# Performance work log

Measured on AMD Instinct MI355X. Metric: run time of the kernel, lower is better.

## Reference

```python
import jax, jax.numpy as jnp
import numpy as np

N_NODES = 100000
N_EDGES = 3200000
IN_C = 256
HID = 32
OUT_C = 64


def setup_inputs() -> dict:
    key = jax.random.key(0)
    ks = jax.random.split(key, 12)
    x = jax.random.normal(ks[0], (N_NODES, IN_C), dtype=jnp.float32)
    edge_index = jax.random.randint(ks[1], (2, N_EDGES), 0, N_NODES, dtype=jnp.int64)

    def lin(kw, kb, fan_in, fan_out):
        bound = 1.0 / np.sqrt(fan_in)
        W = jax.random.uniform(kw, (fan_out, fan_in), jnp.float32, -bound, bound)
        b = jax.random.uniform(kb, (fan_out,), jnp.float32, -bound, bound)
        return W, b

    W0, b0 = lin(ks[2], ks[3], IN_C, HID)
    W1, b1 = lin(ks[4], ks[5], HID, HID)
    W2, b2 = lin(ks[6], ks[7], HID, HID)
    W3, b3 = lin(ks[8], ks[9], HID, HID)
    W4, b4 = lin(ks[10], ks[11], HID, OUT_C)
    return {"x": x, "edge_index": edge_index,
            "W0": W0, "b0": b0, "W1": W1, "b1": b1, "W2": W2, "b2": b2,
            "W3": W3, "b3": b3, "W4": W4, "b4": b4}


def _gcn_norm(edge_index, num_nodes):
    # add self loops, symmetric normalization (PyG gcn_norm, edge_weight = 1)
    loop = jnp.arange(num_nodes, dtype=edge_index.dtype)
    row = jnp.concatenate([edge_index[0], loop])  # source nodes
    col = jnp.concatenate([edge_index[1], loop])  # target nodes
    deg = jax.ops.segment_sum(jnp.ones_like(col, dtype=jnp.float32), col,
                              num_segments=num_nodes)
    dinv = jnp.where(deg > 0, jax.lax.rsqrt(jnp.maximum(deg, 1e-12)), 0.0)
    norm = dinv[row] * dinv[col]
    return row, col, norm


def reference(x, edge_index, W0, b0, W1, b1, W2, b2, W3, b3, W4, b4):
    row, col, norm = _gcn_norm(edge_index, N_NODES)

    def prop(h):
        # gather source features, scale by norm, scatter-add to targets
        return jax.ops.segment_sum(norm[:, None] * h[row], col,
                                   num_segments=N_NODES)

    def sgconv(h, W, b):  # SGConv with K=1: propagate then linear
        return prop(h) @ W.T + b

    h = x @ W0.T + b0
    h = jax.nn.relu(sgconv(h, W1, b1))
    h = jax.nn.relu(sgconv(h, W2, b2))
    h = jax.nn.relu(sgconv(h, W3, b3))
    return h @ W4.T + b4
```

## Files before the change

kernel.cpp:

```cpp
#include <hip/hip_runtime.h>
#include <hip/hip_fp16.h>

#define N_NODES 100000
#define N_EDGES 3200000
#define IN_C 256
#define HID 32
#define OUT_C 64
#define CAP 80
#define NP 100032
#define BINW 256
#define BSH 8
#define NBIN 391
#define BCHUNK 4096
#define CAPB 12288

typedef _Float16 f16x8 __attribute__((ext_vector_type(8)));
typedef float f32x4 __attribute__((ext_vector_type(4)));

__device__ __forceinline__ float dot4(const float4 a, const float4 b) {
    return a.x * b.x + a.y * b.y + a.z * b.z + a.w * b.w;
}

__device__ __forceinline__ float4 h4tof4(uint2 v) {
    __half2 a = *reinterpret_cast<__half2*>(&v.x);
    __half2 b = *reinterpret_cast<__half2*>(&v.y);
    float2 fa = __half22float2(a), fb = __half22float2(b);
    return make_float4(fa.x, fa.y, fb.x, fb.y);
}
__device__ __forceinline__ uint2 f4toh4(float4 f) {
    __half2 a = __float22half2_rn(make_float2(f.x, f.y));
    __half2 b = __float22half2_rn(make_float2(f.z, f.w));
    uint2 v;
    v.x = *reinterpret_cast<unsigned int*>(&a);
    v.y = *reinterpret_cast<unsigned int*>(&b);
    return v;
}

__device__ __forceinline__ void h8acc(uint4 v, float* acc) {
    __half2* p = reinterpret_cast<__half2*>(&v);
    #pragma unroll
    for (int i = 0; i < 4; ++i) {
        float2 f = __half22float2(p[i]);
        acc[2 * i] += f.x;
        acc[2 * i + 1] += f.y;
    }
}

__device__ __forceinline__ unsigned packh2(_Float16 a, _Float16 b) {
    unsigned short ua = __builtin_bit_cast(unsigned short, a);
    unsigned short ub = __builtin_bit_cast(unsigned short, b);
    return (unsigned)ua | ((unsigned)ub << 16);
}


__global__ __launch_bounds__(256) void k_binscatter(const int* __restrict__ row,
                                                    const int* __restrict__ col,
                                                    int* __restrict__ binCursor,
                                                    unsigned* __restrict__ pairs) {
    __shared__ int lcnt[512];
    __shared__ int lofs[512];
    __shared__ int gbase[512];
    __shared__ int sbuf[2][256];
    __shared__ unsigned stage[BCHUNK];
    __shared__ unsigned short sbin[BCHUNK];
    const int t = threadIdx.x;
    for (int i = t; i < 512; i += 256) lcnt[i] = 0;
    __syncthreads();

    const int e0 = blockIdx.x * BCHUNK;
    const int e1 = min(N_EDGES, e0 + BCHUNK);
    const int cn = e1 - e0;

    for (int i = e0 + t; i < e1; i += 256)
        atomicAdd(&lcnt[col[i] >> BSH], 1);
    __syncthreads();

    const int a0 = lcnt[2 * t], a1 = lcnt[2 * t + 1];
    sbuf[0][t] = a0 + a1;
    __syncthreads();
    int s = 0;
    for (int off = 1; off < 256; off <<= 1) {
        int d = s ^ 1;
        int v = sbuf[s][t];
        if (t >= off) v += sbuf[s][t - off];
        sbuf[d][t] = v;
        __syncthreads();
        s = d;
    }
    const int excl = sbuf[s][t] - (a0 + a1);
    lofs[2 * t] = excl;
    lofs[2 * t + 1] = excl + a0;
    __syncthreads();

    for (int i = t; i < 512; i += 256) {
        int c = lcnt[i];
        gbase[i] = c ? atomicAdd(&binCursor[i], c) : 0;
        lcnt[i] = 0;
    }
    __syncthreads();

    for (int i = e0 + t; i < e1; i += 256) {
        int cc = col[i];
        int b = cc >> BSH;
        int p = lofs[b] + atomicAdd(&lcnt[b], 1);
        stage[p] = ((unsigned)row[i] << 8) | (unsigned)(cc & 255);
        sbin[p] = (unsigned short)b;
    }
    __syncthreads();

    for (int i = t; i < cn; i += 256) {
        int b = sbin[i];
        int pos = gbase[b] + (i - lofs[b]);
        if (pos < CAPB)
            pairs[(size_t)b * CAPB + pos] = stage[i];
    }
}

__global__ __launch_bounds__(256) void k_binbuild(const unsigned* __restrict__ pairs,
                                                  const int* __restrict__ binCursor,
                                                  int* __restrict__ bucket,
                                                  int* __restrict__ degc,
                                                  float* __restrict__ dinv) {
    __shared__ int cur[BINW];
    const int t = threadIdx.x;
    const int bin = blockIdx.x;
    const int base = bin * BINW;
    cur[t] = 0;
    __syncthreads();
    const unsigned* __restrict__ slab = pairs + (size_t)bin * CAPB;
    const int cn = min(binCursor[bin], CAPB);
    for (int i = t; i < cn; i += 256) {
        unsigned p = slab[i];
        int c = (int)(p & 255u);
        int pos = atomicAdd(&cur[c], 1);
        if (pos < CAP) bucket[(size_t)(base + c) * CAP + pos] = (int)(p >> 8);
    }
    __syncthreads();
    int n = base + t;
    if (n < N_NODES) {
        int d = cur[t];
        degc[n] = d;
        dinv[n] = 1.0f / sqrtf((float)(d + 1));
    }
}


__global__ void k_hist(const int* __restrict__ col, int* __restrict__ deg) {
    int i = blockIdx.x * 256 + threadIdx.x;
    if (i < N_EDGES) atomicAdd(&deg[col[i]], 1);
}

__global__ void k_scan1(const int* __restrict__ deg, int* __restrict__ rowptr,
                        int* __restrict__ bsum) {
    __shared__ int buf[2][1024];
    const int t = threadIdx.x, b = blockIdx.x;
    const int i = b * 1024 + t;
    int v = (i < N_NODES) ? deg[i] : 0;
    buf[0][t] = v;
    __syncthreads();
    int src = 0;
    for (int off = 1; off < 1024; off <<= 1) {
        int dst = src ^ 1;
        int val = buf[src][t];
        if (t >= off) val += buf[src][t - off];
        buf[dst][t] = val;
        __syncthreads();
        src = dst;
    }
    int incl = buf[src][t];
    if (i < N_NODES) rowptr[i] = incl - v;
    if (t == 1023) bsum[b] = incl;
}

__global__ void k_scan2(int* __restrict__ bsum, int nb) {
    __shared__ int buf[2][128];
    const int t = threadIdx.x;
    int v = (t < nb) ? bsum[t] : 0;
    buf[0][t] = v;
    __syncthreads();
    int src = 0;
    for (int off = 1; off < 128; off <<= 1) {
        int dst = src ^ 1;
        int val = buf[src][t];
        if (t >= off) val += buf[src][t - off];
        buf[dst][t] = val;
        __syncthreads();
        src = dst;
    }
    if (t < nb) bsum[t] = buf[src][t] - v;
}

__global__ void k_scan3(int* __restrict__ rowptr, const int* __restrict__ bsum) {
    int i = blockIdx.x * 256 + threadIdx.x;
    if (i < N_NODES) rowptr[i] += bsum[i >> 10];
}

__global__ void k_dinv(const int* __restrict__ cnt, int stride,
                       float* __restrict__ dinv, int* __restrict__ degc) {
    int i = blockIdx.x * 256 + threadIdx.x;
    if (i < N_NODES) {
        int d = cnt[i * stride];
        degc[i] = d;
        dinv[i] = 1.0f / sqrtf((float)(d + 1));
    }
}

__global__ void k_scatter(const int* __restrict__ row, const int* __restrict__ col,
                          const int* __restrict__ rowptr, int* __restrict__ cursor,
                          int* __restrict__ csr) {
    int i = blockIdx.x * 256 + threadIdx.x;
    if (i < N_EDGES) {
        int c = col[i];
        int pos = rowptr[c] + atomicAdd(&cursor[c], 1);
        csr[pos] = row[i];
    }
}

__global__ __launch_bounds__(256) void k_lin0_mfma(
        const float* __restrict__ x,
        const float* __restrict__ W0,
        const float* __restrict__ b0,
        const float* __restrict__ dinv,
        uint2* __restrict__ g2) {
    __shared__ f16x8 WH[1024];
    __shared__ f16x8 WL[1024];

    const int t = threadIdx.x;
    const int w = t >> 6;
    const int l = t & 63;
    const int lr = l & 15;
    const int lg = l >> 4;

    for (int s = t; s < 1024; s += 256) {
        const int lane = s & 63;
        const int mtks = s >> 6;
        const int ks = mtks & 7, mt = mtks >> 3;
        const float* wr = W0 + (size_t)(mt * 16 + (lane & 15)) * IN_C
                             + ks * 32 + (lane >> 4) * 8;
        float4 a0 = *(const float4*)(wr);
        float4 a1 = *(const float4*)(wr + 4);
        float v[8] = {a0.x, a0.y, a0.z, a0.w, a1.x, a1.y, a1.z, a1.w};
        f16x8 h, lo;
        #pragma unroll
        for (int e = 0; e < 8; ++e) {
            float sv = v[e] * 16.0f;
            _Float16 hh = (_Float16)sv;
            h[e] = hh;
            lo[e] = (_Float16)(sv - (float)hh);
        }
        WH[s] = h;
        WL[s] = lo;
    }
    __syncthreads();

    const int unit = blockIdx.x * 4 + w;
    if (unit * 32 >= N_NODES) return;
    const int n0 = unit * 32;

    f32x4 acc[2][2];
    #pragma unroll
    for (int mt = 0; mt < 2; ++mt)
        #pragma unroll
        for (int nt = 0; nt < 2; ++nt)
            acc[mt][nt] = (f32x4){0.f, 0.f, 0.f, 0.f};

    const float* xr0 = x + (size_t)(n0 + lr) * IN_C + lg * 8;
    const float* xr1 = x + (size_t)(n0 + 16 + lr) * IN_C + lg * 8;

    #pragma unroll
    for (int ks = 0; ks < 8; ++ks) {
        float4 u0 = *(const float4*)(xr0 + ks * 32);
        float4 u1 = *(const float4*)(xr0 + ks * 32 + 4);
        float4 v0 = *(const float4*)(xr1 + ks * 32);
        float4 v1 = *(const float4*)(xr1 + ks * 32 + 4);
        float fu[8] = {u0.x, u0.y, u0.z, u0.w, u1.x, u1.y, u1.z, u1.w};
        float fv[8] = {v0.x, v0.y, v0.z, v0.w, v1.x, v1.y, v1.z, v1.w};
        f16x8 xh0, xl0, xh1, xl1;
        #pragma unroll
        for (int e = 0; e < 8; ++e) {
            _Float16 h0 = (_Float16)fu[e];
            xh0[e] = h0;
            xl0[e] = (_Float16)(fu[e] - (float)h0);
            _Float16 h1 = (_Float16)fv[e];
            xh1[e] = h1;
            xl1[e] = (_Float16)(fv[e] - (float)h1);
        }
        #pragma unroll
        for (int mt = 0; mt < 2; ++mt) {
            f16x8 wh = WH[mt * 512 + ks * 64 + l];
            f16x8 wl = WL[mt * 512 + ks * 64 + l];
            acc[mt][0] = __builtin_amdgcn_mfma_f32_16x16x32_f16(wh, xh0, acc[mt][0], 0, 0, 0);
            acc[mt][0] = __builtin_amdgcn_mfma_f32_16x16x32_f16(wh, xl0, acc[mt][0], 0, 0, 0);
            acc[mt][0] = __builtin_amdgcn_mfma_f32_16x16x32_f16(wl, xh0, acc[mt][0], 0, 0, 0);
            acc[mt][1] = __builtin_amdgcn_mfma_f32_16x16x32_f16(wh, xh1, acc[mt][1], 0, 0, 0);
            acc[mt][1] = __builtin_amdgcn_mfma_f32_16x16x32_f16(wh, xl1, acc[mt][1], 0, 0, 0);
            acc[mt][1] = __builtin_amdgcn_mfma_f32_16x16x32_f16(wl, xh1, acc[mt][1], 0, 0, 0);
        }
    }

    #pragma unroll
    for (int nt = 0; nt < 2; ++nt) {
        const int node = n0 + nt * 16 + lr;
        const float dv = dinv[node];
        #pragma unroll
        for (int mt = 0; mt < 2; ++mt) {
            const float4 bb = *(const float4*)(b0 + mt * 16 + lg * 4);
            f32x4 a = acc[mt][nt];
            float4 r = make_float4((a[0] * 0.0625f + bb.x) * dv,
                                   (a[1] * 0.0625f + bb.y) * dv,
                                   (a[2] * 0.0625f + bb.z) * dv,
                                   (a[3] * 0.0625f + bb.w) * dv);
            g2[(size_t)node * 8 + mt * 4 + lg] = f4toh4(r);
        }
    }
}

__global__ __launch_bounds__(256) void k_prop_mfma(
        const uint2* __restrict__ g2, const int* __restrict__ idx,
        const int* __restrict__ cnt_arr,
        const float* __restrict__ dinv,
        const float* __restrict__ W, const float* __restrict__ b,
        uint2* __restrict__ gout2) {
    __shared__ f16x8 WH[128], WL[128];
    const int t = threadIdx.x;
    if (t < 128) {
        const int lane = t & 63, mt = t >> 6;
        const float* wr = W + (size_t)(mt * 16 + (lane & 15)) * HID + (lane >> 4) * 8;
        f16x8 h, lo;
        #pragma unroll
        for (int e = 0; e < 8; ++e) {
            float sv = wr[e] * 8.0f;
            _Float16 hh = (_Float16)sv;
            h[e] = hh;
            lo[e] = (_Float16)(sv - (float)hh);
        }
        WH[t] = h;
        WL[t] = lo;
    }
    __syncthreads();

    const int l = t & 63;
    const int tile = blockIdx.x * 4 + (t >> 6);
    const int n0 = tile * 16;
    if (n0 >= N_NODES) return;
    const int node = n0 + (l & 15);
    const int lg = l >> 4;

    const uint4* __restrict__ g4 = (const uint4*)g2;
    float acc[8];
    #pragma unroll
    for (int i = 0; i < 8; ++i) acc[i] = 0.f;
    h8acc(g4[(size_t)node * 4 + lg], acc);

    const int cn = min(cnt_arr[node], CAP);
    const int* __restrict__ e = idx + (size_t)node * CAP;
    int j = 0;
    for (; j + 8 <= cn; j += 8) {
        int4 ra = *(const int4*)(e + j);
        int4 rb = *(const int4*)(e + j + 4);
        uint4 v0 = g4[(size_t)ra.x * 4 + lg];
        uint4 v1 = g4[(size_t)ra.y * 4 + lg];
        uint4 v2 = g4[(size_t)ra.z * 4 + lg];
        uint4 v3 = g4[(size_t)ra.w * 4 + lg];
        uint4 v4 = g4[(size_t)rb.x * 4 + lg];
        uint4 v5 = g4[(size_t)rb.y * 4 + lg];
        uint4 v6 = g4[(size_t)rb.z * 4 + lg];
        uint4 v7 = g4[(size_t)rb.w * 4 + lg];
        h8acc(v0, acc); h8acc(v1, acc); h8acc(v2, acc); h8acc(v3, acc);
        h8acc(v4, acc); h8acc(v5, acc); h8acc(v6, acc); h8acc(v7, acc);
    }
    for (; j < cn; ++j) h8acc(g4[(size_t)e[j] * 4 + lg], acc);

    f16x8 bh, bl;
    #pragma unroll
    for (int i = 0; i < 8; ++i) {
        _Float16 hh = (_Float16)acc[i];
        bh[i] = hh;
        bl[i] = (_Float16)(acc[i] - (float)hh);
    }

    f32x4 c0 = (f32x4){0.f, 0.f, 0.f, 0.f};
    f32x4 c1 = (f32x4){0.f, 0.f, 0.f, 0.f};
    {
        f16x8 wh0 = WH[l], wl0 = WL[l];
        f16x8 wh1 = WH[64 + l], wl1 = WL[64 + l];
        c0 = __builtin_amdgcn_mfma_f32_16x16x32_f16(wh0, bh, c0, 0, 0, 0);
        c0 = __builtin_amdgcn_mfma_f32_16x16x32_f16(wh0, bl, c0, 0, 0, 0);
        c0 = __builtin_amdgcn_mfma_f32_16x16x32_f16(wl0, bh, c0, 0, 0, 0);
        c1 = __builtin_amdgcn_mfma_f32_16x16x32_f16(wh1, bh, c1, 0, 0, 0);
        c1 = __builtin_amdgcn_mfma_f32_16x16x32_f16(wh1, bl, c1, 0, 0, 0);
        c1 = __builtin_amdgcn_mfma_f32_16x16x32_f16(wl1, bh, c1, 0, 0, 0);
    }

    const float dv = dinv[node];
    #pragma unroll
    for (int mt = 0; mt < 2; ++mt) {
        const f32x4 bb = *(const f32x4*)(b + mt * 16 + lg * 4);
        f32x4 a = mt ? c1 : c0;
        float4 r;
        r.x = fmaxf(bb[0] + dv * (a[0] * 0.125f), 0.f) * dv;
        r.y = fmaxf(bb[1] + dv * (a[1] * 0.125f), 0.f) * dv;
        r.z = fmaxf(bb[2] + dv * (a[2] * 0.125f), 0.f) * dv;
        r.w = fmaxf(bb[3] + dv * (a[3] * 0.125f), 0.f) * dv;
        gout2[(size_t)node * 8 + mt * 4 + lg] = f4toh4(r);
    }
}

__global__ __launch_bounds__(256) void k_last_mfma(
        const uint2* __restrict__ g2, const int* __restrict__ idx,
        const int* __restrict__ cnt_arr,
        const float* __restrict__ dinv,
        const float* __restrict__ W3, const float* __restrict__ b3,
        const float* __restrict__ W4, const float* __restrict__ b4,
        float4* __restrict__ out4) {
    __shared__ f16x8 WH3[128], WL3[128];
    __shared__ f16x8 WH4[256], WL4[256];
    const int t = threadIdx.x;
    if (t < 128) {
        const int lane = t & 63, mt = t >> 6;
        const float* wr = W3 + (size_t)(mt * 16 + (lane & 15)) * HID + (lane >> 4) * 8;
        f16x8 h, lo;
        #pragma unroll
        for (int e = 0; e < 8; ++e) {
            float sv = wr[e] * 8.0f;
            _Float16 hh = (_Float16)sv;
            h[e] = hh;
            lo[e] = (_Float16)(sv - (float)hh);
        }
        WH3[t] = h;
        WL3[t] = lo;
    }
    {
        const int lane = t & 63, mt = t >> 6;
        const float* wr = W4 + (size_t)(mt * 16 + (lane & 15)) * HID + (lane >> 4) * 8;
        f16x8 h, lo;
        #pragma unroll
        for (int e = 0; e < 8; ++e) {
            float sv = wr[e] * 8.0f;
            _Float16 hh = (_Float16)sv;
            h[e] = hh;
            lo[e] = (_Float16)(sv - (float)hh);
        }
        WH4[t] = h;
        WL4[t] = lo;
    }
    __syncthreads();

    const int l = t & 63;
    const int tile = blockIdx.x * 4 + (t >> 6);
    const int n0 = tile * 16;
    if (n0 >= N_NODES) return;
    const int nl = l & 15;
    const int node = n0 + nl;
    const int lg = l >> 4;

    const uint4* __restrict__ g4 = (const uint4*)g2;
    float acc[8];
    #pragma unroll
    for (int i = 0; i < 8; ++i) acc[i] = 0.f;
    h8acc(g4[(size_t)node * 4 + lg], acc);

    const int cn = min(cnt_arr[node], CAP);
    const int* __restrict__ e = idx + (size_t)node * CAP;
    int j = 0;
    for (; j + 8 <= cn; j += 8) {
        int4 ra = *(const int4*)(e + j);
        int4 rb = *(const int4*)(e + j + 4);
        uint4 v0 = g4[(size_t)ra.x * 4 + lg];
        uint4 v1 = g4[(size_t)ra.y * 4 + lg];
        uint4 v2 = g4[(size_t)ra.z * 4 + lg];
        uint4 v3 = g4[(size_t)ra.w * 4 + lg];
        uint4 v4 = g4[(size_t)rb.x * 4 + lg];
        uint4 v5 = g4[(size_t)rb.y * 4 + lg];
        uint4 v6 = g4[(size_t)rb.z * 4 + lg];
        uint4 v7 = g4[(size_t)rb.w * 4 + lg];
        h8acc(v0, acc); h8acc(v1, acc); h8acc(v2, acc); h8acc(v3, acc);
        h8acc(v4, acc); h8acc(v5, acc); h8acc(v6, acc); h8acc(v7, acc);
    }
    for (; j < cn; ++j) h8acc(g4[(size_t)e[j] * 4 + lg], acc);

    f16x8 bh, bl;
    #pragma unroll
    for (int i = 0; i < 8; ++i) {
        _Float16 hh = (_Float16)acc[i];
        bh[i] = hh;
        bl[i] = (_Float16)(acc[i] - (float)hh);
    }

    f32x4 c0 = (f32x4){0.f, 0.f, 0.f, 0.f};
    f32x4 c1 = (f32x4){0.f, 0.f, 0.f, 0.f};
    {
        f16x8 wh0 = WH3[l], wl0 = WL3[l];
        f16x8 wh1 = WH3[64 + l], wl1 = WL3[64 + l];
        c0 = __builtin_amdgcn_mfma_f32_16x16x32_f16(wh0, bh, c0, 0, 0, 0);
        c0 = __builtin_amdgcn_mfma_f32_16x16x32_f16(wh0, bl, c0, 0, 0, 0);
        c0 = __builtin_amdgcn_mfma_f32_16x16x32_f16(wl0, bh, c0, 0, 0, 0);
        c1 = __builtin_amdgcn_mfma_f32_16x16x32_f16(wh1, bh, c1, 0, 0, 0);
        c1 = __builtin_amdgcn_mfma_f32_16x16x32_f16(wh1, bl, c1, 0, 0, 0);
        c1 = __builtin_amdgcn_mfma_f32_16x16x32_f16(wl1, bh, c1, 0, 0, 0);
    }

    const float dv = dinv[node];
    const f32x4 b3a = *(const f32x4*)(b3 + lg * 4);
    const f32x4 b3b = *(const f32x4*)(b3 + 16 + lg * 4);
    float h0[4], h1[4];
    #pragma unroll
    for (int r = 0; r < 4; ++r) {
        h0[r] = fmaxf(b3a[r] + dv * (c0[r] * 0.125f), 0.f);
        h1[r] = fmaxf(b3b[r] + dv * (c1[r] * 0.125f), 0.f);
    }

    unsigned ph[2][2], pl_[2][2];
    #pragma unroll
    for (int p = 0; p < 2; ++p) {
        _Float16 a0 = (_Float16)h0[2 * p], a1 = (_Float16)h0[2 * p + 1];
        _Float16 l0 = (_Float16)(h0[2 * p] - (float)a0);
        _Float16 l1 = (_Float16)(h0[2 * p + 1] - (float)a1);
        ph[0][p] = packh2(a0, a1);
        pl_[0][p] = packh2(l0, l1);
        _Float16 c0_ = (_Float16)h1[2 * p], c1_ = (_Float16)h1[2 * p + 1];
        _Float16 d0 = (_Float16)(h1[2 * p] - (float)c0_);
        _Float16 d1 = (_Float16)(h1[2 * p + 1] - (float)c1_);
        ph[1][p] = packh2(c0_, c1_);
        pl_[1][p] = packh2(d0, d1);
    }

    union { unsigned u[4]; f16x8 v; } Bh, Bl;
    #pragma unroll
    for (int q = 0; q < 4; ++q) {
        int src = nl + 16 * ((lg & 1) * 2 + (q >> 1));
        unsigned a0 = (unsigned)__shfl((int)ph[0][q & 1], src, 64);
        unsigned a1 = (unsigned)__shfl((int)ph[1][q & 1], src, 64);
        Bh.u[q] = (lg >= 2) ? a1 : a0;
        unsigned c0_ = (unsigned)__shfl((int)pl_[0][q & 1], src, 64);
        unsigned c1_ = (unsigned)__shfl((int)pl_[1][q & 1], src, 64);
        Bl.u[q] = (lg >= 2) ? c1_ : c0_;
    }

    f32x4 o0 = (f32x4){0.f, 0.f, 0.f, 0.f};
    f32x4 o1 = (f32x4){0.f, 0.f, 0.f, 0.f};
    f32x4 o2 = (f32x4){0.f, 0.f, 0.f, 0.f};
    f32x4 o3 = (f32x4){0.f, 0.f, 0.f, 0.f};
    {
        f16x8 wh, wl;
        wh = WH4[l];        wl = WL4[l];
        o0 = __builtin_amdgcn_mfma_f32_16x16x32_f16(wh, Bh.v, o0, 0, 0, 0);
        o0 = __builtin_amdgcn_mfma_f32_16x16x32_f16(wh, Bl.v, o0, 0, 0, 0);
        o0 = __builtin_amdgcn_mfma_f32_16x16x32_f16(wl, Bh.v, o0, 0, 0, 0);
        wh = WH4[64 + l];   wl = WL4[64 + l];
        o1 = __builtin_amdgcn_mfma_f32_16x16x32_f16(wh, Bh.v, o1, 0, 0, 0);
        o1 = __builtin_amdgcn_mfma_f32_16x16x32_f16(wh, Bl.v, o1, 0, 0, 0);
        o1 = __builtin_amdgcn_mfma_f32_16x16x32_f16(wl, Bh.v, o1, 0, 0, 0);
        wh = WH4[128 + l];  wl = WL4[128 + l];
        o2 = __builtin_amdgcn_mfma_f32_16x16x32_f16(wh, Bh.v, o2, 0, 0, 0);
        o2 = __builtin_amdgcn_mfma_f32_16x16x32_f16(wh, Bl.v, o2, 0, 0, 0);
        o2 = __builtin_amdgcn_mfma_f32_16x16x32_f16(wl, Bh.v, o2, 0, 0, 0);
        wh = WH4[192 + l];  wl = WL4[192 + l];
        o3 = __builtin_amdgcn_mfma_f32_16x16x32_f16(wh, Bh.v, o3, 0, 0, 0);
        o3 = __builtin_amdgcn_mfma_f32_16x16x32_f16(wh, Bl.v, o3, 0, 0, 0);
        o3 = __builtin_amdgcn_mfma_f32_16x16x32_f16(wl, Bh.v, o3, 0, 0, 0);
    }

    #pragma unroll
    for (int mt = 0; mt < 4; ++mt) {
        const f32x4 bb = *(const f32x4*)(b4 + mt * 16 + lg * 4);
        f32x4 a = (mt == 0) ? o0 : (mt == 1) ? o1 : (mt == 2) ? o2 : o3;
        out4[(size_t)node * 16 + mt * 4 + lg] =
            make_float4(a[0] * 0.125f + bb[0], a[1] * 0.125f + bb[1],
                        a[2] * 0.125f + bb[2], a[3] * 0.125f + bb[3]);
    }
}


__global__ __launch_bounds__(256) void k_prop2(
        const uint2* __restrict__ g2, const int* __restrict__ idx,
        const int* __restrict__ base_arr,
        const int* __restrict__ cnt_arr, int maxcnt,
        const float* __restrict__ dinv,
        const float* __restrict__ W, const float* __restrict__ b,
        uint2* __restrict__ gout2) {
    __shared__ float4 Ws[HID * 9];
    const int t = threadIdx.x;
    { int c = t >> 3, k4 = t & 7; Ws[c * 9 + k4] = ((const float4*)W)[t]; }
    __syncthreads();

    const int l = t & 7;
    const int n = blockIdx.x * 32 + (t >> 3);
    if (n >= N_NODES) return;

    int cnt = cnt_arr[n];
    if (cnt > maxcnt) cnt = maxcnt;
    const int base = base_arr[n];
    const int* __restrict__ e = idx + base;

    float4 acc = h4tof4(g2[n * 8 + l]);
    int j = 0;
    for (; j + 8 <= cnt; j += 8) {
        int r0 = e[j], r1 = e[j + 1], r2 = e[j + 2], r3 = e[j + 3];
        int r4 = e[j + 4], r5 = e[j + 5], r6 = e[j + 6], r7 = e[j + 7];
        uint2 v0 = g2[r0 * 8 + l], v1 = g2[r1 * 8 + l];
        uint2 v2 = g2[r2 * 8 + l], v3 = g2[r3 * 8 + l];
        uint2 v4 = g2[r4 * 8 + l], v5 = g2[r5 * 8 + l];
        uint2 v6 = g2[r6 * 8 + l], v7 = g2[r7 * 8 + l];
        float4 a0 = h4tof4(v0), a1 = h4tof4(v1), a2 = h4tof4(v2), a3 = h4tof4(v3);
        float4 a4 = h4tof4(v4), a5 = h4tof4(v5), a6 = h4tof4(v6), a7 = h4tof4(v7);
        acc.x += a0.x + a1.x + a2.x + a3.x + a4.x + a5.x + a6.x + a7.x;
        acc.y += a0.y + a1.y + a2.y + a3.y + a4.y + a5.y + a6.y + a7.y;
        acc.z += a0.z + a1.z + a2.z + a3.z + a4.z + a5.z + a6.z + a7.z;
        acc.w += a0.w + a1.w + a2.w + a3.w + a4.w + a5.w + a6.w + a7.w;
    }
    for (; j < cnt; ++j) {
        float4 a = h4tof4(g2[e[j] * 8 + l]);
        acc.x += a.x; acc.y += a.y; acc.z += a.z; acc.w += a.w;
    }

    const float dv = dinv[n];
    float4 y = make_float4(0.f, 0.f, 0.f, 0.f);
    #pragma unroll
    for (int m = 0; m < 8; ++m) {
        float4 sv;
        sv.x = __shfl(acc.x, m, 8);
        sv.y = __shfl(acc.y, m, 8);
        sv.z = __shfl(acc.z, m, 8);
        sv.w = __shfl(acc.w, m, 8);
        y.x += dot4(Ws[(4 * l + 0) * 9 + m], sv);
        y.y += dot4(Ws[(4 * l + 1) * 9 + m], sv);
        y.z += dot4(Ws[(4 * l + 2) * 9 + m], sv);
        y.w += dot4(Ws[(4 * l + 3) * 9 + m], sv);
    }
    const float4 bb = ((const float4*)b)[l];
    y.x = fmaxf(bb.x + dv * y.x, 0.f) * dv;
    y.y = fmaxf(bb.y + dv * y.y, 0.f) * dv;
    y.z = fmaxf(bb.z + dv * y.z, 0.f) * dv;
    y.w = fmaxf(bb.w + dv * y.w, 0.f) * dv;
    gout2[n * 8 + l] = f4toh4(y);
}

__global__ __launch_bounds__(256) void k_last2(
        const uint2* __restrict__ g2, const int* __restrict__ idx,
        const int* __restrict__ base_arr,
        const int* __restrict__ cnt_arr, int maxcnt,
        const float* __restrict__ dinv,
        const float* __restrict__ W3, const float* __restrict__ b3,
        const float* __restrict__ W4, const float* __restrict__ b4,
        float4* __restrict__ out4) {
    __shared__ float4 W3s[HID * 9];
    __shared__ float4 W4s[OUT_C * 9];
    const int t = threadIdx.x;
    { int c = t >> 3, k4 = t & 7; W3s[c * 9 + k4] = ((const float4*)W3)[t]; }
    #pragma unroll
    for (int f = t; f < 512; f += 256) {
        int c = f >> 3, k4 = f & 7;
        W4s[c * 9 + k4] = ((const float4*)W4)[f];
    }
    __syncthreads();

    const int l = t & 7;
    const int n = blockIdx.x * 32 + (t >> 3);
    if (n >= N_NODES) return;

    int cnt = cnt_arr[n];
    if (cnt > maxcnt) cnt = maxcnt;
    const int base = base_arr[n];
    const int* __restrict__ e = idx + base;

    float4 acc = h4tof4(g2[n * 8 + l]);
    int j = 0;
    for (; j + 8 <= cnt; j += 8) {
        int r0 = e[j], r1 = e[j + 1], r2 = e[j + 2], r3 = e[j + 3];
        int r4 = e[j + 4], r5 = e[j + 5], r6 = e[j + 6], r7 = e[j + 7];
        uint2 v0 = g2[r0 * 8 + l], v1 = g2[r1 * 8 + l];
        uint2 v2 = g2[r2 * 8 + l], v3 = g2[r3 * 8 + l];
        uint2 v4 = g2[r4 * 8 + l], v5 = g2[r5 * 8 + l];
        uint2 v6 = g2[r6 * 8 + l], v7 = g2[r7 * 8 + l];
        float4 a0 = h4tof4(v0), a1 = h4tof4(v1), a2 = h4tof4(v2), a3 = h4tof4(v3);
        float4 a4 = h4tof4(v4), a5 = h4tof4(v5), a6 = h4tof4(v6), a7 = h4tof4(v7);
        acc.x += a0.x + a1.x + a2.x + a3.x + a4.x + a5.x + a6.x + a7.x;
        acc.y += a0.y + a1.y + a2.y + a3.y + a4.y + a5.y + a6.y + a7.y;
        acc.z += a0.z + a1.z + a2.z + a3.z + a4.z + a5.z + a6.z + a7.z;
        acc.w += a0.w + a1.w + a2.w + a3.w + a4.w + a5.w + a6.w + a7.w;
    }
    for (; j < cnt; ++j) {
        float4 a = h4tof4(g2[e[j] * 8 + l]);
        acc.x += a.x; acc.y += a.y; acc.z += a.z; acc.w += a.w;
    }

    const float dv = dinv[n];
    float4 y = make_float4(0.f, 0.f, 0.f, 0.f);
    #pragma unroll
    for (int m = 0; m < 8; ++m) {
        float4 sv;
        sv.x = __shfl(acc.x, m, 8);
        sv.y = __shfl(acc.y, m, 8);
        sv.z = __shfl(acc.z, m, 8);
        sv.w = __shfl(acc.w, m, 8);
        y.x += dot4(W3s[(4 * l + 0) * 9 + m], sv);
        y.y += dot4(W3s[(4 * l + 1) * 9 + m], sv);
        y.z += dot4(W3s[(4 * l + 2) * 9 + m], sv);
        y.w += dot4(W3s[(4 * l + 3) * 9 + m], sv);
    }
    const float4 b3v = ((const float4*)b3)[l];
    float4 h;
    h.x = fmaxf(b3v.x + dv * y.x, 0.f);
    h.y = fmaxf(b3v.y + dv * y.y, 0.f);
    h.z = fmaxf(b3v.z + dv * y.z, 0.f);
    h.w = fmaxf(b3v.w + dv * y.w, 0.f);

    float4 ya = make_float4(0.f, 0.f, 0.f, 0.f);
    float4 yb = make_float4(0.f, 0.f, 0.f, 0.f);
    #pragma unroll
    for (int m = 0; m < 8; ++m) {
        float4 hv;
        hv.x = __shfl(h.x, m, 8);
        hv.y = __shfl(h.y, m, 8);
        hv.z = __shfl(h.z, m, 8);
        hv.w = __shfl(h.w, m, 8);
        ya.x += dot4(W4s[(4 * l + 0) * 9 + m], hv);
        ya.y += dot4(W4s[(4 * l + 1) * 9 + m], hv);
        ya.z += dot4(W4s[(4 * l + 2) * 9 + m], hv);
        ya.w += dot4(W4s[(4 * l + 3) * 9 + m], hv);
        yb.x += dot4(W4s[(32 + 4 * l + 0) * 9 + m], hv);
        yb.y += dot4(W4s[(32 + 4 * l + 1) * 9 + m], hv);
        yb.z += dot4(W4s[(32 + 4 * l + 2) * 9 + m], hv);
        yb.w += dot4(W4s[(32 + 4 * l + 3) * 9 + m], hv);
    }
    const float4 b4a = ((const float4*)b4)[l];
    const float4 b4b = ((const float4*)b4)[8 + l];
    ya.x += b4a.x; ya.y += b4a.y; ya.z += b4a.z; ya.w += b4a.w;
    yb.x += b4b.x; yb.y += b4b.y; yb.z += b4b.z; yb.w += b4b.w;
    out4[n * 16 + l] = ya;
    out4[n * 16 + 8 + l] = yb;
}


extern "C" void kernel_launch(void* const* d_in, const int* in_sizes, int n_in,
                              void* d_out, int out_size, void* d_ws, size_t ws_size,
                              hipStream_t stream) {
    const float* x   = (const float*)d_in[0];
    const int*   ei  = (const int*)d_in[1];
    const int*   row = ei;
    const int*   col = ei + N_EDGES;
    const float* W0 = (const float*)d_in[2];
    const float* b0 = (const float*)d_in[3];
    const float* W1 = (const float*)d_in[4];
    const float* b1 = (const float*)d_in[5];
    const float* W2 = (const float*)d_in[6];
    const float* b2 = (const float*)d_in[7];
    const float* W3 = (const float*)d_in[8];
    const float* b3 = (const float*)d_in[9];
    const float* W4 = (const float*)d_in[10];
    const float* b4 = (const float*)d_in[11];
    float* out = (float*)d_out;

    const int EB = (N_EDGES + 255) / 256;
    const int NB256 = (N_NODES + 255) / 256;
    const int NB1024 = (N_NODES + 1023) / 1024;
    const int CB = (N_EDGES + BCHUNK - 1) / BCHUNK;
    const int UNITS = (N_NODES + 31) / 32;
    const int LB0 = (UNITS + 3) / 4;
    const int MB = (N_NODES + 63) / 64;
    const int PB2 = (N_NODES + 31) / 32;

    const size_t SLAB_BYTES = (size_t)NBIN * CAPB * 4;
    const size_t G_BYTES = 2ull * NP * 8 * 8;
    const size_t UNION_BYTES = SLAB_BYTES > G_BYTES ? SLAB_BYTES : G_BYTES;
    const size_t FAST_BYTES =
        (size_t)N_NODES * CAP * 4 + 2ull * NP * 4 + 3ull * 512 * 4 + UNION_BYTES;

    if (ws_size >= FAST_BYTES) {
        int*   bucket    = (int*)d_ws;
        float* dinv      = (float*)(bucket + (size_t)N_NODES * CAP);
        int*   degc      = (int*)(dinv + NP);
        int*   binCnt    = degc + NP;
        int*   binStart  = binCnt + 512;
        int*   binCursor = binStart + 512;
        char*  uni       = (char*)(binCursor + 512);
        unsigned* pairs  = (unsigned*)uni;
        uint2* gA        = (uint2*)uni;
        uint2* gB        = gA + (size_t)NP * 4 * 2;

        hipMemsetAsync(binCursor, 0, 512 * sizeof(int), stream);
        k_binscatter<<<CB, 256, 0, stream>>>(row, col, binCursor, pairs);
        k_binbuild<<<NBIN, 256, 0, stream>>>(pairs, binCursor,
                                             bucket, degc, dinv);

        k_lin0_mfma<<<LB0, 256, 0, stream>>>(x, W0, b0, dinv, gA);

        k_prop_mfma<<<MB, 256, 0, stream>>>(gA, bucket, degc, dinv, W1, b1, gB);
        k_prop_mfma<<<MB, 256, 0, stream>>>(gB, bucket, degc, dinv, W2, b2, gA);
        k_last_mfma<<<MB, 256, 0, stream>>>(gA, bucket, degc, dinv,
                                            W3, b3, W4, b4, (float4*)out);
    } else {
        int*   deg    = (int*)d_ws;
        int*   rowptr = deg + NP;
        int*   cursor = rowptr + NP;
        int*   bsum   = cursor + NP;
        float* dinv   = (float*)(bsum + 128);
        int*   csr    = (int*)(dinv + NP);
        uint2* gA     = (uint2*)(csr + N_EDGES);
        uint2* gB     = gA + (size_t)N_NODES * 8;

        hipMemsetAsync(deg, 0, (size_t)NP * 3 * sizeof(int), stream);
        k_hist<<<EB, 256, 0, stream>>>(col, deg);
        k_scan1<<<NB1024, 1024, 0, stream>>>(deg, rowptr, bsum);
        k_scan2<<<1, 128, 0, stream>>>(bsum, NB1024);
        k_scan3<<<NB256, 256, 0, stream>>>(rowptr, bsum);
        k_dinv<<<NB256, 256, 0, stream>>>(deg, 1, dinv, cursor);
        hipMemsetAsync(cursor, 0, (size_t)NP * sizeof(int), stream);
        k_scatter<<<EB, 256, 0, stream>>>(row, col, rowptr, cursor, csr);

        k_lin0_mfma<<<LB0, 256, 0, stream>>>(x, W0, b0, dinv, gA);

        k_prop2<<<PB2, 256, 0, stream>>>(gA, csr, rowptr, deg, 1 << 30,
                                         dinv, W1, b1, gB);
        k_prop2<<<PB2, 256, 0, stream>>>(gB, csr, rowptr, deg, 1 << 30,
                                         dinv, W2, b2, gA);
        k_last2<<<PB2, 256, 0, stream>>>(gA, csr, rowptr, deg, 1 << 30,
                                         dinv, W3, b3, W4, b4, (float4*)out);
    }
}
```

Measured before the change: 413.3 us.

## Split hidden features into two half-planes for phased neighbor gather

Stores the fp16 hidden features as two separate planes (channels 0-15 and 16-31) instead of one interleaved 64-byte row. The propagation kernels now gather the low plane first and then the high plane, with lanes splitting even and odd edges and combining them by cross-lane shuffle. The aim is to halve the gather footprint in each phase so it stays resident in L2/MALL. The cost is reading the edge index list twice per node, an extra block barrier, and added shuffle work.

Result: slower. 455.1 us (+10.1%).

```diff
diff --git a/kernel.cpp b/kernel.cpp
--- a/kernel.cpp
+++ b/kernel.cpp
@@ -221,7 +221,7 @@
         const float* __restrict__ W0,
         const float* __restrict__ b0,
         const float* __restrict__ dinv,
-        uint2* __restrict__ g2) {
+        uint2* __restrict__ gLo, uint2* __restrict__ gHi, int ns) {
     __shared__ f16x8 WH[1024];
     __shared__ f16x8 WL[1024];
 
@@ -310,17 +310,45 @@
                                    (a[1] * 0.0625f + bb.y) * dv,
                                    (a[2] * 0.0625f + bb.z) * dv,
                                    (a[3] * 0.0625f + bb.w) * dv);
-            g2[(size_t)node * 8 + mt * 4 + lg] = f4toh4(r);
+            uint2* dst = mt ? gHi : gLo;
+            dst[(size_t)node * ns + lg] = f4toh4(r);
         }
     }
 }
 
-__global__ __launch_bounds__(256) void k_prop_mfma(
-        const uint2* __restrict__ g2, const int* __restrict__ idx,
-        const int* __restrict__ cnt_arr,
+
+__device__ __forceinline__ void pull_gather(const uint4* __restrict__ plane,
+                                            const int* __restrict__ e, int cn,
+                                            int part, int eo, float* a) {
+    int j = 0;
+    for (; j + 8 <= cn; j += 8) {
+        int4 ea = *(const int4*)(e + j);
+        int4 eb = *(const int4*)(e + j + 4);
+        int r0 = eo ? ea.y : ea.x;
+        int r1 = eo ? ea.w : ea.z;
+        int r2 = eo ? eb.y : eb.x;
+        int r3 = eo ? eb.w : eb.z;
+        uint4 v0 = plane[(size_t)r0 * 2 + part];
+        uint4 v1 = plane[(size_t)r1 * 2 + part];
+        uint4 v2 = plane[(size_t)r2 * 2 + part];
+        uint4 v3 = plane[(size_t)r3 * 2 + part];
+        h8acc(v0, a); h8acc(v1, a); h8acc(v2, a); h8acc(v3, a);
+    }
+    for (; j + 2 <= cn; j += 2) {
+        int r = e[j + eo];
+        h8acc(plane[(size_t)r * 2 + part], a);
+    }
+    if (j < cn && eo == 0) {
+        h8acc(plane[(size_t)e[j] * 2 + part], a);
+    }
+}
+
+__global__ __launch_bounds__(256) void k_prop_ph(
+        const uint4* __restrict__ planeLo, const uint4* __restrict__ planeHi,
+        const int* __restrict__ bucket, const int* __restrict__ degc,
         const float* __restrict__ dinv,
         const float* __restrict__ W, const float* __restrict__ b,
-        uint2* __restrict__ gout2) {
+        uint2* __restrict__ outLo, uint2* __restrict__ outHi) {
     __shared__ f16x8 WH[128], WL[128];
     const int t = threadIdx.x;
     if (t < 128) {
@@ -341,42 +369,42 @@
 
     const int l = t & 63;
     const int tile = blockIdx.x * 4 + (t >> 6);
-    const int n0 = tile * 16;
-    if (n0 >= N_NODES) return;
-    const int node = n0 + (l & 15);
+    const int node = tile * 16 + (l & 15);
+    const int nsafe = min(node, N_NODES - 1);
     const int lg = l >> 4;
-
-    const uint4* __restrict__ g4 = (const uint4*)g2;
-    float acc[8];
-    #pragma unroll
-    for (int i = 0; i < 8; ++i) acc[i] = 0.f;
-    h8acc(g4[(size_t)node * 4 + lg], acc);
-
-    const int cn = min(cnt_arr[node], CAP);
-    const int* __restrict__ e = idx + (size_t)node * CAP;
-    int j = 0;
-    for (; j + 8 <= cn; j += 8) {
-        int4 ra = *(const int4*)(e + j);
-        int4 rb = *(const int4*)(e + j + 4);
-        uint4 v0 = g4[(size_t)ra.x * 4 + lg];
-        uint4 v1 = g4[(size_t)ra.y * 4 + lg];
-        uint4 v2 = g4[(size_t)ra.z * 4 + lg];
-        uint4 v3 = g4[(size_t)ra.w * 4 + lg];
-        uint4 v4 = g4[(size_t)rb.x * 4 + lg];
-        uint4 v5 = g4[(size_t)rb.y * 4 + lg];
-        uint4 v6 = g4[(size_t)rb.z * 4 + lg];
-        uint4 v7 = g4[(size_t)rb.w * 4 + lg];
-        h8acc(v0, acc); h8acc(v1, acc); h8acc(v2, acc); h8acc(v3, acc);
-        h8acc(v4, acc); h8acc(v5, acc); h8acc(v6, acc); h8acc(v7, acc);
-    }
-    for (; j < cn; ++j) h8acc(g4[(size_t)e[j] * 4 + lg], acc);
+    const int part = lg & 1, eo = lg >> 1;
+
+    const int cn = min(degc[nsafe], CAP);
+    const int* __restrict__ e = bucket + (size_t)nsafe * CAP;
+
+    float aLo[8];
+    #pragma unroll
+    for (int i = 0; i < 8; ++i) aLo[i] = 0.f;
+    if (lg < 2) h8acc(planeLo[(size_t)nsafe * 2 + part], aLo);
+    pull_gather(planeLo, e, cn, part, eo, aLo);
+    #pragma unroll
+    for (int i = 0; i < 8; ++i) aLo[i] += __shfl_xor(aLo[i], 32, 64);
+
+    __syncthreads();
+
+    float aHi[8];
+    #pragma unroll
+    for (int i = 0; i < 8; ++i) aHi[i] = 0.f;
+    if (lg < 2) h8acc(planeHi[(size_t)nsafe * 2 + part], aHi);
+    pull_gather(planeHi, e, cn, part, eo, aHi);
+    #pragma unroll
+    for (int i = 0; i < 8; ++i) aHi[i] += __shfl_xor(aHi[i], 32, 64);
+
+    float av[8];
+    #pragma unroll
+    for (int i = 0; i < 8; ++i) av[i] = (lg < 2) ? aLo[i] : aHi[i];
 
     f16x8 bh, bl;
     #pragma unroll
     for (int i = 0; i < 8; ++i) {
-        _Float16 hh = (_Float16)acc[i];
+        _Float16 hh = (_Float16)av[i];
         bh[i] = hh;
-        bl[i] = (_Float16)(acc[i] - (float)hh);
+        bl[i] = (_Float16)(av[i] - (float)hh);
     }
 
     f32x4 c0 = (f32x4){0.f, 0.f, 0.f, 0.f};
@@ -392,23 +420,26 @@
         c1 = __builtin_amdgcn_mfma_f32_16x16x32_f16(wl1, bh, c1, 0, 0, 0);
     }
 
-    const float dv = dinv[node];
-    #pragma unroll
-    for (int mt = 0; mt < 2; ++mt) {
-        const f32x4 bb = *(const f32x4*)(b + mt * 16 + lg * 4);
-        f32x4 a = mt ? c1 : c0;
-        float4 r;
-        r.x = fmaxf(bb[0] + dv * (a[0] * 0.125f), 0.f) * dv;
-        r.y = fmaxf(bb[1] + dv * (a[1] * 0.125f), 0.f) * dv;
-        r.z = fmaxf(bb[2] + dv * (a[2] * 0.125f), 0.f) * dv;
-        r.w = fmaxf(bb[3] + dv * (a[3] * 0.125f), 0.f) * dv;
-        gout2[(size_t)node * 8 + mt * 4 + lg] = f4toh4(r);
-    }
-}
-
-__global__ __launch_bounds__(256) void k_last_mfma(
-        const uint2* __restrict__ g2, const int* __restrict__ idx,
-        const int* __restrict__ cnt_arr,
+    if (node < N_NODES) {
+        const float dv = dinv[node];
+        #pragma unroll
+        for (int mt = 0; mt < 2; ++mt) {
+            const f32x4 bb = *(const f32x4*)(b + mt * 16 + lg * 4);
+            f32x4 aa = mt ? c1 : c0;
+            float4 r;
+            r.x = fmaxf(bb[0] + dv * (aa[0] * 0.125f), 0.f) * dv;
+            r.y = fmaxf(bb[1] + dv * (aa[1] * 0.125f), 0.f) * dv;
+            r.z = fmaxf(bb[2] + dv * (aa[2] * 0.125f), 0.f) * dv;
+            r.w = fmaxf(bb[3] + dv * (aa[3] * 0.125f), 0.f) * dv;
+            uint2* dst = mt ? outHi : outLo;
+            dst[(size_t)node * 4 + lg] = f4toh4(r);
+        }
+    }
+}
+
+__global__ __launch_bounds__(256) void k_last_ph(
+        const uint4* __restrict__ planeLo, const uint4* __restrict__ planeHi,
+        const int* __restrict__ bucket, const int* __restrict__ degc,
         const float* __restrict__ dinv,
         const float* __restrict__ W3, const float* __restrict__ b3,
         const float* __restrict__ W4, const float* __restrict__ b4,
@@ -448,43 +479,43 @@
 
     const int l = t & 63;
     const int tile = blockIdx.x * 4 + (t >> 6);
-    const int n0 = tile * 16;
-    if (n0 >= N_NODES) return;
     const int nl = l & 15;
-    const int node = n0 + nl;
+    const int node = tile * 16 + nl;
+    const int nsafe = min(node, N_NODES - 1);
     const int lg = l >> 4;
-
-    const uint4* __restrict__ g4 = (const uint4*)g2;
-    float acc[8];
-    #pragma unroll
-    for (int i = 0; i < 8; ++i) acc[i] = 0.f;
-    h8acc(g4[(size_t)node * 4 + lg], acc);
-
-    const int cn = min(cnt_arr[node], CAP);
-    const int* __restrict__ e = idx + (size_t)node * CAP;
-    int j = 0;
-    for (; j + 8 <= cn; j += 8) {
-        int4 ra = *(const int4*)(e + j);
-        int4 rb = *(const int4*)(e + j + 4);
-        uint4 v0 = g4[(size_t)ra.x * 4 + lg];
-        uint4 v1 = g4[(size_t)ra.y * 4 + lg];
-        uint4 v2 = g4[(size_t)ra.z * 4 + lg];
-        uint4 v3 = g4[(size_t)ra.w * 4 + lg];
-        uint4 v4 = g4[(size_t)rb.x * 4 + lg];
-        uint4 v5 = g4[(size_t)rb.y * 4 + lg];
-        uint4 v6 = g4[(size_t)rb.z * 4 + lg];
-        uint4 v7 = g4[(size_t)rb.w * 4 + lg];
-        h8acc(v0, acc); h8acc(v1, acc); h8acc(v2, acc); h8acc(v3, acc);
-        h8acc(v4, acc); h8acc(v5, acc); h8acc(v6, acc); h8acc(v7, acc);
-    }
-    for (; j < cn; ++j) h8acc(g4[(size_t)e[j] * 4 + lg], acc);
+    const int part = lg & 1, eo = lg >> 1;
+
+    const int cn = min(degc[nsafe], CAP);
+    const int* __restrict__ e = bucket + (size_t)nsafe * CAP;
+
+    float aLo[8];
+    #pragma unroll
+    for (int i = 0; i < 8; ++i) aLo[i] = 0.f;
+    if (lg < 2) h8acc(planeLo[(size_t)nsafe * 2 + part], aLo);
+    pull_gather(planeLo, e, cn, part, eo, aLo);
+    #pragma unroll
+    for (int i = 0; i < 8; ++i) aLo[i] += __shfl_xor(aLo[i], 32, 64);
+
+    __syncthreads();
+
+    float aHi[8];
+    #pragma unroll
+    for (int i = 0; i < 8; ++i) aHi[i] = 0.f;
+    if (lg < 2) h8acc(planeHi[(size_t)nsafe * 2 + part], aHi);
+    pull_gather(planeHi, e, cn, part, eo, aHi);
+    #pragma unroll
+    for (int i = 0; i < 8; ++i) aHi[i] += __shfl_xor(aHi[i], 32, 64);
+
+    float av[8];
+    #pragma unroll
+    for (int i = 0; i < 8; ++i) av[i] = (lg < 2) ? aLo[i] : aHi[i];
 
     f16x8 bh, bl;
     #pragma unroll
     for (int i = 0; i < 8; ++i) {
-        _Float16 hh = (_Float16)acc[i];
+        _Float16 hh = (_Float16)av[i];
         bh[i] = hh;
-        bl[i] = (_Float16)(acc[i] - (float)hh);
+        bl[i] = (_Float16)(av[i] - (float)hh);
     }
 
     f32x4 c0 = (f32x4){0.f, 0.f, 0.f, 0.f};
@@ -500,7 +531,7 @@
         c1 = __builtin_amdgcn_mfma_f32_16x16x32_f16(wl1, bh, c1, 0, 0, 0);
     }
 
-    const float dv = dinv[node];
+    const float dv = dinv[nsafe];
     const f32x4 b3a = *(const f32x4*)(b3 + lg * 4);
     const f32x4 b3b = *(const f32x4*)(b3 + 16 + lg * 4);
     float h0[4], h1[4];
@@ -561,13 +592,15 @@
         o3 = __builtin_amdgcn_mfma_f32_16x16x32_f16(wl, Bh.v, o3, 0, 0, 0);
     }
 
-    #pragma unroll
-    for (int mt = 0; mt < 4; ++mt) {
-        const f32x4 bb = *(const f32x4*)(b4 + mt * 16 + lg * 4);
-        f32x4 a = (mt == 0) ? o0 : (mt == 1) ? o1 : (mt == 2) ? o2 : o3;
-        out4[(size_t)node * 16 + mt * 4 + lg] =
-            make_float4(a[0] * 0.125f + bb[0], a[1] * 0.125f + bb[1],
-                        a[2] * 0.125f + bb[2], a[3] * 0.125f + bb[3]);
+    if (node < N_NODES) {
+        #pragma unroll
+        for (int mt = 0; mt < 4; ++mt) {
+            const f32x4 bb = *(const f32x4*)(b4 + mt * 16 + lg * 4);
+            f32x4 aa = (mt == 0) ? o0 : (mt == 1) ? o1 : (mt == 2) ? o2 : o3;
+            out4[(size_t)node * 16 + mt * 4 + lg] =
+                make_float4(aa[0] * 0.125f + bb[0], aa[1] * 0.125f + bb[1],
+                            aa[2] * 0.125f + bb[2], aa[3] * 0.125f + bb[3]);
+        }
     }
 }
 
@@ -761,9 +794,10 @@
     const int MB = (N_NODES + 63) / 64;
     const int PB2 = (N_NODES + 31) / 32;
 
+    const size_t PLANE_U2 = (size_t)NP * 4;
     const size_t SLAB_BYTES = (size_t)NBIN * CAPB * 4;
-    const size_t G_BYTES = 2ull * NP * 8 * 8;
-    const size_t UNION_BYTES = SLAB_BYTES > G_BYTES ? SLAB_BYTES : G_BYTES;
+    const size_t PLANES_BYTES = 4ull * PLANE_U2 * 8;
+    const size_t UNION_BYTES = SLAB_BYTES > PLANES_BYTES ? SLAB_BYTES : PLANES_BYTES;
     const size_t FAST_BYTES =
         (size_t)N_NODES * CAP * 4 + 2ull * NP * 4 + 3ull * 512 * 4 + UNION_BYTES;
 
@@ -776,20 +810,25 @@
         int*   binCursor = binStart + 512;
         char*  uni       = (char*)(binCursor + 512);
         unsigned* pairs  = (unsigned*)uni;
-        uint2* gA        = (uint2*)uni;
-        uint2* gB        = gA + (size_t)NP * 4 * 2;
+        uint2* gAlo = (uint2*)uni;
+        uint2* gAhi = gAlo + PLANE_U2;
+        uint2* gBlo = gAhi + PLANE_U2;
+        uint2* gBhi = gBlo + PLANE_U2;
 
         hipMemsetAsync(binCursor, 0, 512 * sizeof(int), stream);
         k_binscatter<<<CB, 256, 0, stream>>>(row, col, binCursor, pairs);
         k_binbuild<<<NBIN, 256, 0, stream>>>(pairs, binCursor,
                                              bucket, degc, dinv);
 
-        k_lin0_mfma<<<LB0, 256, 0, stream>>>(x, W0, b0, dinv, gA);
-
-        k_prop_mfma<<<MB, 256, 0, stream>>>(gA, bucket, degc, dinv, W1, b1, gB);
-        k_prop_mfma<<<MB, 256, 0, stream>>>(gB, bucket, degc, dinv, W2, b2, gA);
-        k_last_mfma<<<MB, 256, 0, stream>>>(gA, bucket, degc, dinv,
-                                            W3, b3, W4, b4, (float4*)out);
+        k_lin0_mfma<<<LB0, 256, 0, stream>>>(x, W0, b0, dinv, gAlo, gAhi, 4);
+
+        k_prop_ph<<<MB, 256, 0, stream>>>((const uint4*)gAlo, (const uint4*)gAhi,
+                                          bucket, degc, dinv, W1, b1, gBlo, gBhi);
+        k_prop_ph<<<MB, 256, 0, stream>>>((const uint4*)gBlo, (const uint4*)gBhi,
+                                          bucket, degc, dinv, W2, b2, gAlo, gAhi);
+        k_last_ph<<<MB, 256, 0, stream>>>((const uint4*)gAlo, (const uint4*)gAhi,
+                                          bucket, degc, dinv,
+                                          W3, b3, W4, b4, (float4*)out);
     } else {
         int*   deg    = (int*)d_ws;
         int*   rowptr = deg + NP;
@@ -809,7 +848,7 @@
         hipMemsetAsync(cursor, 0, (size_t)NP * sizeof(int), stream);
         k_scatter<<<EB, 256, 0, stream>>>(row, col, rowptr, cursor, csr);
 
-        k_lin0_mfma<<<LB0, 256, 0, stream>>>(x, W0, b0, dinv, gA);
+        k_lin0_mfma<<<LB0, 256, 0, stream>>>(x, W0, b0, dinv, gA, gA + 4, 8);
 
         k_prop2<<<PB2, 256, 0, stream>>>(gA, csr, rowptr, deg, 1 << 30,
                                          dinv, W1, b1, gB);
```
